# Performance work log

Measured on AMD Instinct MI355X. Metric: run time of the kernel, lower is better.

## Reference

```python
import jax, jax.numpy as jnp
import numpy as np

B, S, D = 4, 2048, 1024


def setup_inputs() -> dict:
    key = jax.random.key(0)
    ks = jax.random.split(key, 11)
    sc = 0.02
    f32 = jnp.float32
    return {
        "x1": jax.random.normal(ks[0], (B, S, D), f32),
        "x2": jax.random.normal(ks[1], (B, S, D), f32),
        "x3": jax.random.normal(ks[2], (B, S, D), f32),
        # Stacked per-modality projection weights, stored (in, out) so y = x @ W + b
        "Wq": jax.random.normal(ks[3], (3, D, D), f32) * sc,
        "bq": jax.random.normal(ks[4], (3, D), f32) * sc,
        "Wk": jax.random.normal(ks[5], (3, D, D), f32) * sc,
        "bk": jax.random.normal(ks[6], (3, D), f32) * sc,
        "Wv": jax.random.normal(ks[7], (3, D, D), f32) * sc,
        "bv": jax.random.normal(ks[8], (3, D), f32) * sc,
        "Wo": jax.random.normal(ks[9], (3, 2 * D, D), f32) * sc,
        "bo": jax.random.normal(ks[10], (3, D), f32) * sc,
    }


def reference(x1, x2, x3, Wq, bq, Wk, bk, Wv, bv, Wo, bo):
    x = jnp.stack([x1, x2, x3])                      # (3, B, S, D)
    q = jnp.einsum('mbsd,mde->mbse', x, Wq) + bq[:, None, None, :]
    k = jnp.einsum('mbsd,mde->mbse', x, Wk) + bk[:, None, None, :]
    v = jnp.einsum('mbsd,mde->mbse', x, Wv) + bv[:, None, None, :]
    scale = 1.0 / jnp.sqrt(jnp.asarray(x.shape[-1], x.dtype))
    # self-scores per modality: q_i @ k_i^T
    scores = jnp.einsum('mbsd,mbtd->mbst', q, k) * scale   # (3, B, S, S)
    attn = jax.nn.softmax(scores, axis=-1)
    # context_i = attn_i @ v_{(i+1) mod 3}  (1->2, 2->3, 3->1); dropout is eval-mode identity
    v_next = jnp.roll(v, shift=-1, axis=0)
    ctx = jnp.einsum('mbst,mbtd->mbsd', attn, v_next)      # (3, B, S, D)
    comb = jnp.concatenate([x, ctx], axis=-1)              # (3, B, S, 2D)
    out = jnp.einsum('mbsf,mfd->mbsd', comb, Wo) + bo[:, None, None, :]
    global_feature = jnp.concatenate([out[0], out[1], out[2]], axis=1)  # (B, 3S, D)
    return out[0], out[1], out[2], global_feature
```

## Files before the change

kernel.cpp:

```cpp
#include <hip/hip_runtime.h>
#include <hip/hip_bf16.h>

typedef __bf16 bf16_t;
typedef __bf16 bf16x8 __attribute__((ext_vector_type(8)));
typedef float f32x4 __attribute__((ext_vector_type(4)));

typedef __attribute__((address_space(1))) unsigned int as1_uint;
typedef __attribute__((address_space(3))) unsigned int as3_uint;

#define Bsz 4
#define Ssz 2048
#define Dsz 1024
#define BSD (Bsz * Ssz * Dsz)
#define SCALE_ 0.03125f

__device__ __forceinline__ void gll16(const void* g, void* l) {
  __builtin_amdgcn_global_load_lds((const as1_uint*)g, (as3_uint*)l, 16, 0, 0);
}

__device__ __forceinline__ void gemm_core(const bf16_t* A, const bf16_t* A2, int ksplit,
                                          int lda, int lda2,
                                          const bf16_t* Bt, int ldb,
                                          int ktiles, f32x4 acc[4][4]) {
  __shared__ __attribute__((aligned(16))) bf16_t As[128 * 64];
  __shared__ __attribute__((aligned(16))) bf16_t Bs[128 * 64];
  const int tid = threadIdx.x;
  const int wave = tid >> 6, lane = tid & 63;
  const int quad = lane >> 4, m16 = lane & 15, x7 = lane & 7;
  const int waveM = (wave >> 1) << 6, waveN = (wave & 1) << 6;
  const int srow = tid >> 3;
  const int schunk = (tid & 7) ^ ((tid >> 3) & 7);
  char* AsB = (char*)As;
  char* BsB = (char*)Bs;
  const int ldsbase = wave << 10;

  for (int kt = 0; kt < ktiles; ++kt) {
    const bf16_t* Ak = (kt < ksplit) ? (A + kt * 64) : (A2 + (kt - ksplit) * 64);
    const int ldak = (kt < ksplit) ? lda : lda2;
    const bf16_t* Bk = Bt + kt * 64;
    __syncthreads();
#pragma unroll
    for (int it = 0; it < 4; ++it)
      gll16(Ak + (size_t)(it * 32 + srow) * ldak + schunk * 8, AsB + it * 4096 + ldsbase);
#pragma unroll
    for (int it = 0; it < 4; ++it)
      gll16(Bk + (size_t)(it * 32 + srow) * ldb + schunk * 8, BsB + it * 4096 + ldsbase);
    __syncthreads();
#pragma unroll
    for (int t = 0; t < 2; ++t) {
      bf16x8 a[4], b[4];
      const int cc = t * 4 + quad;
#pragma unroll
      for (int i = 0; i < 4; ++i) {
        const int rr = waveM + i * 16 + m16;
        a[i] = *(const bf16x8*)(AsB + rr * 128 + ((cc ^ x7) << 4));
      }
#pragma unroll
      for (int j = 0; j < 4; ++j) {
        const int rr = waveN + j * 16 + m16;
        b[j] = *(const bf16x8*)(BsB + rr * 128 + ((cc ^ x7) << 4));
      }
#pragma unroll
      for (int i = 0; i < 4; ++i)
#pragma unroll
        for (int j = 0; j < 4; ++j)
          acc[i][j] = __builtin_amdgcn_mfma_f32_16x16x32_bf16(a[i], b[j], acc[i][j], 0, 0, 0);
    }
  }
}

__global__ __launch_bounds__(256, 2)
void gemm_bt_bf16(const bf16_t* __restrict__ A, long long sAz, int lda,
                  const bf16_t* __restrict__ Bt, long long sBz, int ldb,
                  const float* __restrict__ bias, int sbz,
                  bf16_t* __restrict__ C, long long sCz, int ldc,
                  int K, int rollB) {
  const int z = blockIdx.z;
  int zb = z;
  if (rollB) { const int m = z >> 2, b = z & 3; zb = ((m + 1) % 3) * Bsz + b; }
  const bf16_t* Az = A + (long long)z * sAz + (size_t)blockIdx.y * 128 * lda;
  const bf16_t* Bz = Bt + (long long)zb * sBz + (size_t)blockIdx.x * 128 * ldb;
  f32x4 acc[4][4];
  const f32x4 zero = {0.f, 0.f, 0.f, 0.f};
#pragma unroll
  for (int i = 0; i < 4; ++i)
#pragma unroll
    for (int j = 0; j < 4; ++j) acc[i][j] = zero;

  gemm_core(Az, Az, 1 << 30, lda, lda, Bz, ldb, K / 64, acc);

  const int lane = threadIdx.x & 63, wave = threadIdx.x >> 6;
  const int m0 = blockIdx.y * 128 + ((wave >> 1) << 6) + ((lane >> 4) << 2);
  const int n0 = blockIdx.x * 128 + ((wave & 1) << 6) + (lane & 15);
  bf16_t* Cz = C + (long long)z * sCz;
  const float* bz = bias ? (bias + (long long)z * sbz) : nullptr;
#pragma unroll
  for (int j = 0; j < 4; ++j) {
    const int col = n0 + j * 16;
    const float bv = bz ? bz[col] : 0.0f;
#pragma unroll
    for (int i = 0; i < 4; ++i) {
      const int row = m0 + i * 16;
#pragma unroll
      for (int r = 0; r < 4; ++r)
        Cz[(size_t)(row + r) * ldc + col] = (bf16_t)(acc[i][j][r] + bv);
    }
  }
}

__global__ __launch_bounds__(256, 2)
void gemm_out(const bf16_t* __restrict__ xb, const bf16_t* __restrict__ ctx,
              const bf16_t* __restrict__ Wot, const float* __restrict__ bo,
              float* __restrict__ out) {
  const int m = blockIdx.z;
  const bf16_t* Az = xb + (long long)m * BSD + (size_t)blockIdx.y * 128 * Dsz;
  const bf16_t* A2z = ctx + (long long)m * BSD + (size_t)blockIdx.y * 128 * Dsz;
  const bf16_t* Bz = Wot + (long long)m * (Dsz * 2 * Dsz) + (size_t)blockIdx.x * 128 * (2 * Dsz);
  f32x4 acc[4][4];
  const f32x4 zero = {0.f, 0.f, 0.f, 0.f};
#pragma unroll
  for (int i = 0; i < 4; ++i)
#pragma unroll
    for (int j = 0; j < 4; ++j) acc[i][j] = zero;

  gemm_core(Az, A2z, 16, Dsz, Dsz, Bz, 2 * Dsz, 32, acc);

  const int lane = threadIdx.x & 63, wave = threadIdx.x >> 6;
  const int m0 = blockIdx.y * 128 + ((wave >> 1) << 6) + ((lane >> 4) << 2);
  const int n0 = blockIdx.x * 128 + ((wave & 1) << 6) + (lane & 15);
  const float* bz = bo + m * Dsz;
#pragma unroll
  for (int j = 0; j < 4; ++j) {
    const int col = n0 + j * 16;
    const float bv = bz[col];
#pragma unroll
    for (int i = 0; i < 4; ++i) {
#pragma unroll
      for (int r = 0; r < 4; ++r) {
        const int row = m0 + i * 16 + r;
        const float v = acc[i][j][r] + bv;
        const int b = row >> 11, s = row & 2047;
        out[(size_t)m * BSD + (size_t)row * Dsz + col] = v;
        out[(size_t)3 * BSD + (size_t)b * (3 * Ssz * Dsz) + (size_t)(m * Ssz + s) * Dsz + col] = v;
      }
    }
  }
}

__global__ __launch_bounds__(256)
void cvt_x(const float* __restrict__ x1, const float* __restrict__ x2,
           const float* __restrict__ x3, bf16_t* __restrict__ xb) {
  const size_t i = ((size_t)blockIdx.x * 256 + threadIdx.x) * 4;
  const float* src;
  size_t off;
  if (i < (size_t)BSD)          { src = x1; off = i; }
  else if (i < (size_t)2 * BSD) { src = x2; off = i - BSD; }
  else                          { src = x3; off = i - (size_t)2 * BSD; }
  const float4 v = *(const float4*)(src + off);
  union { bf16_t h[4]; uint2 u; } o;
  o.h[0] = (bf16_t)v.x; o.h[1] = (bf16_t)v.y; o.h[2] = (bf16_t)v.z; o.h[3] = (bf16_t)v.w;
  *(uint2*)(xb + i) = o.u;
}

template <typename TIN>
__global__ __launch_bounds__(256)
void transpose_to_bf16(const TIN* __restrict__ in, bf16_t* __restrict__ out,
                       int ldin, int ldout, long long sIn, long long sOut) {
  __shared__ bf16_t Ts[64][65];
  const int t = threadIdx.x;
  const long long z = blockIdx.z;
  const TIN* inz = in + z * sIn;
  bf16_t* outz = out + z * sOut;
  const int r0 = blockIdx.y << 6, c0 = blockIdx.x << 6;
#pragma unroll
  for (int e = 0; e < 4; ++e) {
    const int idx = (e * 256 + t) * 4;
    const int rr = idx >> 6, cc = idx & 63;
    const TIN* p = inz + (size_t)(r0 + rr) * ldin + (c0 + cc);
    if constexpr (sizeof(TIN) == 4) {
      const float4 v = *(const float4*)p;
      Ts[rr][cc] = (bf16_t)v.x; Ts[rr][cc + 1] = (bf16_t)v.y;
      Ts[rr][cc + 2] = (bf16_t)v.z; Ts[rr][cc + 3] = (bf16_t)v.w;
    } else {
      union { bf16_t h[4]; uint2 u; } tmp;
      tmp.u = *(const uint2*)p;
      Ts[rr][cc] = tmp.h[0]; Ts[rr][cc + 1] = tmp.h[1];
      Ts[rr][cc + 2] = tmp.h[2]; Ts[rr][cc + 3] = tmp.h[3];
    }
  }
  __syncthreads();
#pragma unroll
  for (int e = 0; e < 4; ++e) {
    const int idx = (e * 256 + t) * 4;
    const int oc = idx >> 6, orr = idx & 63;
    union { bf16_t h[4]; uint2 u; } o4;
    o4.h[0] = Ts[orr][oc]; o4.h[1] = Ts[orr + 1][oc];
    o4.h[2] = Ts[orr + 2][oc]; o4.h[3] = Ts[orr + 3][oc];
    *(uint2*)(outz + (size_t)(c0 + oc) * ldout + (r0 + orr)) = o4.u;
  }
}

__device__ __forceinline__ unsigned bfbits(float f) {
  union { bf16_t h; unsigned short u; } c;
  c.h = (bf16_t)f;
  return (unsigned)c.u;
}

__global__ __launch_bounds__(256)
void softmax_rows(bf16_t* __restrict__ Sc) {
  const size_t row = blockIdx.x;
  uint4* p = (uint4*)(Sc + row * Ssz);
  const int t = threadIdx.x;
  const int lane = t & 63, wave = t >> 6;
  uint4 u = p[t];
  float v[8];
  v[0] = __uint_as_float(u.x << 16); v[1] = __uint_as_float(u.x & 0xffff0000u);
  v[2] = __uint_as_float(u.y << 16); v[3] = __uint_as_float(u.y & 0xffff0000u);
  v[4] = __uint_as_float(u.z << 16); v[5] = __uint_as_float(u.z & 0xffff0000u);
  v[6] = __uint_as_float(u.w << 16); v[7] = __uint_as_float(u.w & 0xffff0000u);

  float mx = v[0];
#pragma unroll
  for (int i = 1; i < 8; ++i) mx = fmaxf(mx, v[i]);
  for (int o = 32; o > 0; o >>= 1) mx = fmaxf(mx, __shfl_xor(mx, o));
  __shared__ float redm[4], reds[4];
  if (lane == 0) redm[wave] = mx;
  __syncthreads();
  mx = fmaxf(fmaxf(redm[0], redm[1]), fmaxf(redm[2], redm[3]));

  float s = 0.f;
#pragma unroll
  for (int i = 0; i < 8; ++i) { v[i] = __expf((v[i] - mx) * SCALE_); s += v[i]; }
  for (int o = 32; o > 0; o >>= 1) s += __shfl_xor(s, o);
  if (lane == 0) reds[wave] = s;
  __syncthreads();
  s = reds[0] + reds[1] + reds[2] + reds[3];
  const float inv = 1.0f / s;
#pragma unroll
  for (int i = 0; i < 8; ++i) v[i] *= inv;

  u.x = bfbits(v[0]) | (bfbits(v[1]) << 16);
  u.y = bfbits(v[2]) | (bfbits(v[3]) << 16);
  u.z = bfbits(v[4]) | (bfbits(v[5]) << 16);
  u.w = bfbits(v[6]) | (bfbits(v[7]) << 16);
  p[t] = u;
}

extern "C" void kernel_launch(void* const* d_in, const int* in_sizes, int n_in,
                              void* d_out, int out_size, void* d_ws, size_t ws_size,
                              hipStream_t stream) {
  const float* x1 = (const float*)d_in[0];
  const float* x2 = (const float*)d_in[1];
  const float* x3 = (const float*)d_in[2];
  const float* Wq = (const float*)d_in[3];
  const float* bq = (const float*)d_in[4];
  const float* Wk = (const float*)d_in[5];
  const float* bk = (const float*)d_in[6];
  const float* Wv = (const float*)d_in[7];
  const float* bv = (const float*)d_in[8];
  const float* Wo = (const float*)d_in[9];
  const float* bo = (const float*)d_in[10];

  char* ws = (char*)d_ws;
  bf16_t* xb  = (bf16_t*)(ws + 0);
  bf16_t* Wqt = (bf16_t*)(ws + 50331648);
  bf16_t* Wkt = (bf16_t*)(ws + 56623104);
  bf16_t* Wvt = (bf16_t*)(ws + 62914560);
  bf16_t* Wot = (bf16_t*)(ws + 69206016);
  bf16_t* Q   = (bf16_t*)(ws + 81788928);
  bf16_t* Kb  = (bf16_t*)(ws + 132120576);
  bf16_t* V   = (bf16_t*)(ws + 182452224);
  bf16_t* Sc  = (bf16_t*)d_out;
  bf16_t* Vt  = Q;
  bf16_t* ctx = Kb;

  cvt_x<<<24576, 256, 0, stream>>>(x1, x2, x3, xb);
  transpose_to_bf16<float><<<dim3(16, 16, 3), 256, 0, stream>>>(Wq, Wqt, 1024, 1024, 1048576LL, 1048576LL);
  transpose_to_bf16<float><<<dim3(16, 16, 3), 256, 0, stream>>>(Wk, Wkt, 1024, 1024, 1048576LL, 1048576LL);
  transpose_to_bf16<float><<<dim3(16, 16, 3), 256, 0, stream>>>(Wv, Wvt, 1024, 1024, 1048576LL, 1048576LL);
  transpose_to_bf16<float><<<dim3(16, 32, 3), 256, 0, stream>>>(Wo, Wot, 1024, 2048, 2097152LL, 2097152LL);
  const dim3 gqkv(8, 64, 3);
  gemm_bt_bf16<<<gqkv, 256, 0, stream>>>(xb, (long long)BSD, Dsz, Wqt, 1048576LL, Dsz, bq, Dsz, Q,  (long long)BSD, Dsz, Dsz, 0);
  gemm_bt_bf16<<<gqkv, 256, 0, stream>>>(xb, (long long)BSD, Dsz, Wkt, 1048576LL, Dsz, bk, Dsz, Kb, (long long)BSD, Dsz, Dsz, 0);
  gemm_bt_bf16<<<gqkv, 256, 0, stream>>>(xb, (long long)BSD, Dsz, Wvt, 1048576LL, Dsz, bv, Dsz, V,  (long long)BSD, Dsz, Dsz, 0);
  gemm_bt_bf16<<<dim3(16, 16, 12), 256, 0, stream>>>(Q, 2097152LL, Dsz, Kb, 2097152LL, Dsz, nullptr, 0, Sc, 4194304LL, Ssz, Dsz, 0);
  softmax_rows<<<24576, 256, 0, stream>>>(Sc);
  transpose_to_bf16<bf16_t><<<dim3(16, 32, 12), 256, 0, stream>>>(V, Vt, 1024, 2048, 2097152LL, 2097152LL);
  gemm_bt_bf16<<<dim3(8, 16, 12), 256, 0, stream>>>(Sc, 4194304LL, Ssz, Vt, 2097152LL, Ssz, nullptr, 0, ctx, 2097152LL, Dsz, Ssz, 1);
  gemm_out<<<dim3(8, 64, 3), 256, 0, stream>>>(xb, ctx, Wot, bo, (float*)d_out);
}
```

Baseline: 950.0 us.

## Fuse QKV projections into one GEMM with transposed V epilogue and vectorized stores

Concatenates the transposed Q/K/V weights per modality so a single launch computes all three projections, and writes V already transposed through shared memory, removing the separate V transpose kernel. Swaps the MFMA operand order so each lane holds four consecutive output columns, which lets all GEMM epilogues use vectorized 8-byte bf16 and 16-byte float stores in place of scalar stores. This costs extra shared memory and a sync in the V path, and changes the workspace buffer aliasing.

```diff
diff --git a/kernel.cpp b/kernel.cpp
--- a/kernel.cpp
+++ b/kernel.cpp
@@ -18,20 +18,23 @@
   __builtin_amdgcn_global_load_lds((const as1_uint*)g, (as3_uint*)l, 16, 0, 0);
 }
 
-__device__ __forceinline__ void gemm_core(const bf16_t* A, const bf16_t* A2, int ksplit,
+__device__ __forceinline__ unsigned bfbits(float f) {
+  union { bf16_t h; unsigned short u; } c;
+  c.h = (bf16_t)f;
+  return (unsigned)c.u;
+}
+
+__device__ __forceinline__ void gemm_core(char* AsB, char* BsB,
+                                          const bf16_t* A, const bf16_t* A2, int ksplit,
                                           int lda, int lda2,
                                           const bf16_t* Bt, int ldb,
                                           int ktiles, f32x4 acc[4][4]) {
-  __shared__ __attribute__((aligned(16))) bf16_t As[128 * 64];
-  __shared__ __attribute__((aligned(16))) bf16_t Bs[128 * 64];
   const int tid = threadIdx.x;
   const int wave = tid >> 6, lane = tid & 63;
   const int quad = lane >> 4, m16 = lane & 15, x7 = lane & 7;
   const int waveM = (wave >> 1) << 6, waveN = (wave & 1) << 6;
   const int srow = tid >> 3;
   const int schunk = (tid & 7) ^ ((tid >> 3) & 7);
-  char* AsB = (char*)As;
-  char* BsB = (char*)Bs;
   const int ldsbase = wave << 10;
 
   for (int kt = 0; kt < ktiles; ++kt) {
@@ -64,17 +67,26 @@
       for (int i = 0; i < 4; ++i)
 #pragma unroll
         for (int j = 0; j < 4; ++j)
-          acc[i][j] = __builtin_amdgcn_mfma_f32_16x16x32_bf16(a[i], b[j], acc[i][j], 0, 0, 0);
-    }
-  }
+          acc[i][j] = __builtin_amdgcn_mfma_f32_16x16x32_bf16(b[j], a[i], acc[i][j], 0, 0, 0);
+    }
+  }
+}
+
+__device__ __forceinline__ ushort4 pack4(const f32x4 v, const float4 b) {
+  ushort4 u;
+  u.x = (unsigned short)bfbits(v[0] + b.x);
+  u.y = (unsigned short)bfbits(v[1] + b.y);
+  u.z = (unsigned short)bfbits(v[2] + b.z);
+  u.w = (unsigned short)bfbits(v[3] + b.w);
+  return u;
 }
 
 __global__ __launch_bounds__(256, 2)
 void gemm_bt_bf16(const bf16_t* __restrict__ A, long long sAz, int lda,
                   const bf16_t* __restrict__ Bt, long long sBz, int ldb,
-                  const float* __restrict__ bias, int sbz,
                   bf16_t* __restrict__ C, long long sCz, int ldc,
                   int K, int rollB) {
+  __shared__ __attribute__((aligned(16))) char smem[32768];
   const int z = blockIdx.z;
   int zb = z;
   if (rollB) { const int m = z >> 2, b = z & 3; zb = ((m + 1) % 3) * Bsz + b; }
@@ -87,23 +99,89 @@
 #pragma unroll
     for (int j = 0; j < 4; ++j) acc[i][j] = zero;
 
-  gemm_core(Az, Az, 1 << 30, lda, lda, Bz, ldb, K / 64, acc);
+  gemm_core(smem, smem + 16384, Az, Az, 1 << 30, lda, lda, Bz, ldb, K / 64, acc);
 
   const int lane = threadIdx.x & 63, wave = threadIdx.x >> 6;
-  const int m0 = blockIdx.y * 128 + ((wave >> 1) << 6) + ((lane >> 4) << 2);
-  const int n0 = blockIdx.x * 128 + ((wave & 1) << 6) + (lane & 15);
+  const int Mb = blockIdx.y * 128 + ((wave >> 1) << 6) + (lane & 15);
+  const int Nb = blockIdx.x * 128 + ((wave & 1) << 6) + ((lane >> 4) << 2);
   bf16_t* Cz = C + (long long)z * sCz;
-  const float* bz = bias ? (bias + (long long)z * sbz) : nullptr;
-#pragma unroll
-  for (int j = 0; j < 4; ++j) {
-    const int col = n0 + j * 16;
-    const float bv = bz ? bz[col] : 0.0f;
-#pragma unroll
-    for (int i = 0; i < 4; ++i) {
-      const int row = m0 + i * 16;
-#pragma unroll
-      for (int r = 0; r < 4; ++r)
-        Cz[(size_t)(row + r) * ldc + col] = (bf16_t)(acc[i][j][r] + bv);
+  const float4 zb4 = {0.f, 0.f, 0.f, 0.f};
+#pragma unroll
+  for (int i = 0; i < 4; ++i) {
+    const int M = Mb + i * 16;
+#pragma unroll
+    for (int j = 0; j < 4; ++j) {
+      const int N = Nb + j * 16;
+      *(ushort4*)(Cz + (size_t)M * ldc + N) = pack4(acc[i][j], zb4);
+    }
+  }
+}
+
+__global__ __launch_bounds__(256, 2)
+void gemm_qkv(const bf16_t* __restrict__ xb, const bf16_t* __restrict__ Wqkvt,
+              const float* __restrict__ bq, const float* __restrict__ bk,
+              const float* __restrict__ bvp,
+              bf16_t* __restrict__ Q, bf16_t* __restrict__ Kb, bf16_t* __restrict__ Vt) {
+  __shared__ __attribute__((aligned(16))) char smem[34048];
+  const int m = blockIdx.z;
+  const int x = blockIdx.x;
+  const int which = x >> 3;
+  const bf16_t* Az = xb + (size_t)m * BSD + (size_t)blockIdx.y * 128 * Dsz;
+  const bf16_t* Bz = Wqkvt + (size_t)m * 3145728 + (size_t)x * 131072;
+  f32x4 acc[4][4];
+  const f32x4 zero = {0.f, 0.f, 0.f, 0.f};
+#pragma unroll
+  for (int i = 0; i < 4; ++i)
+#pragma unroll
+    for (int j = 0; j < 4; ++j) acc[i][j] = zero;
+
+  gemm_core(smem, smem + 16384, Az, Az, 1 << 30, Dsz, Dsz, Bz, Dsz, 16, acc);
+
+  const int tid = threadIdx.x;
+  const int lane = tid & 63, wave = tid >> 6;
+  const int Ml = ((wave >> 1) << 6) + (lane & 15);
+  const int Nl = ((wave & 1) << 6) + ((lane >> 4) << 2);
+  const int dseg0 = (x & 7) * 128;
+  const float* bb = (which == 0 ? bq : which == 1 ? bk : bvp) + m * Dsz;
+
+  if (which < 2) {
+    bf16_t* Cz = (which == 0 ? Q : Kb) + (size_t)m * BSD;
+#pragma unroll
+    for (int j = 0; j < 4; ++j) {
+      const int N = Nl + j * 16;
+      const float4 b4 = *(const float4*)(bb + dseg0 + N);
+#pragma unroll
+      for (int i = 0; i < 4; ++i) {
+        const int M = blockIdx.y * 128 + Ml + i * 16;
+        *(ushort4*)(Cz + (size_t)M * Dsz + dseg0 + N) = pack4(acc[i][j], b4);
+      }
+    }
+  } else {
+    unsigned short* T = (unsigned short*)smem;
+    __syncthreads();
+#pragma unroll
+    for (int j = 0; j < 4; ++j) {
+      const int N = Nl + j * 16;
+      const float4 b4 = *(const float4*)(bb + dseg0 + N);
+      const float bia[4] = {b4.x, b4.y, b4.z, b4.w};
+#pragma unroll
+      for (int i = 0; i < 4; ++i) {
+        const int M = Ml + i * 16;
+#pragma unroll
+        for (int r = 0; r < 4; ++r)
+          T[(N + r) * 132 + M] = (unsigned short)bfbits(acc[i][j][r] + bia[r]);
+      }
+    }
+    __syncthreads();
+    const int b = blockIdx.y >> 4;
+    const int s0 = (blockIdx.y & 15) * 128;
+    bf16_t* Vz = Vt + ((size_t)(m * 4 + b) * 1024 + dseg0) * Ssz;
+#pragma unroll
+    for (int e = 0; e < 16; ++e) {
+      const int idx = e * 256 + tid;
+      const int nl = idx >> 5, mc = (idx & 31) * 4;
+      const ushort4 u = *(const ushort4*)(T + nl * 132 + mc);
+      *(ushort4*)(Vz + (size_t)nl * Ssz + s0 + mc) = u;
     }
   }
 }
@@ -112,10 +190,11 @@
 void gemm_out(const bf16_t* __restrict__ xb, const bf16_t* __restrict__ ctx,
               const bf16_t* __restrict__ Wot, const float* __restrict__ bo,
               float* __restrict__ out) {
+  __shared__ __attribute__((aligned(16))) char smem[32768];
   const int m = blockIdx.z;
-  const bf16_t* Az = xb + (long long)m * BSD + (size_t)blockIdx.y * 128 * Dsz;
-  const bf16_t* A2z = ctx + (long long)m * BSD + (size_t)blockIdx.y * 128 * Dsz;
-  const bf16_t* Bz = Wot + (long long)m * (Dsz * 2 * Dsz) + (size_t)blockIdx.x * 128 * (2 * Dsz);
+  const bf16_t* Az = xb + (size_t)m * BSD + (size_t)blockIdx.y * 128 * Dsz;
+  const bf16_t* A2z = ctx + (size_t)m * BSD + (size_t)blockIdx.y * 128 * Dsz;
+  const bf16_t* Bz = Wot + (size_t)m * (Dsz * 2 * Dsz) + (size_t)blockIdx.x * 128 * (2 * Dsz);
   f32x4 acc[4][4];
   const f32x4 zero = {0.f, 0.f, 0.f, 0.f};
 #pragma unroll
@@ -123,26 +202,27 @@
 #pragma unroll
     for (int j = 0; j < 4; ++j) acc[i][j] = zero;
 
-  gemm_core(Az, A2z, 16, Dsz, Dsz, Bz, 2 * Dsz, 32, acc);
+  gemm_core(smem, smem + 16384, Az, A2z, 16, Dsz, Dsz, Bz, 2 * Dsz, 32, acc);
 
   const int lane = threadIdx.x & 63, wave = threadIdx.x >> 6;
-  const int m0 = blockIdx.y * 128 + ((wave >> 1) << 6) + ((lane >> 4) << 2);
-  const int n0 = blockIdx.x * 128 + ((wave & 1) << 6) + (lane & 15);
+  const int Mb = blockIdx.y * 128 + ((wave >> 1) << 6) + (lane & 15);
+  const int Nb = blockIdx.x * 128 + ((wave & 1) << 6) + ((lane >> 4) << 2);
   const float* bz = bo + m * Dsz;
 #pragma unroll
-  for (int j = 0; j < 4; ++j) {
-    const int col = n0 + j * 16;
-    const float bv = bz[col];
-#pragma unroll
-    for (int i = 0; i < 4; ++i) {
-#pragma unroll
-      for (int r = 0; r < 4; ++r) {
-        const int row = m0 + i * 16 + r;
-        const float v = acc[i][j][r] + bv;
-        const int b = row >> 11, s = row & 2047;
-        out[(size_t)m * BSD + (size_t)row * Dsz + col] = v;
-        out[(size_t)3 * BSD + (size_t)b * (3 * Ssz * Dsz) + (size_t)(m * Ssz + s) * Dsz + col] = v;
-      }
+  for (int i = 0; i < 4; ++i) {
+    const int M = Mb + i * 16;
+    const int b = M >> 11, s = M & 2047;
+    float* o1 = out + (size_t)m * BSD + (size_t)M * Dsz;
+    float* o2 = out + (size_t)3 * BSD + (size_t)b * (3 * Ssz * Dsz) + (size_t)(m * Ssz + s) * Dsz;
+#pragma unroll
+    for (int j = 0; j < 4; ++j) {
+      const int N = Nb + j * 16;
+      const float4 b4 = *(const float4*)(bz + N);
+      float4 o;
+      o.x = acc[i][j][0] + b4.x; o.y = acc[i][j][1] + b4.y;
+      o.z = acc[i][j][2] + b4.z; o.w = acc[i][j][3] + b4.w;
+      *(float4*)(o1 + N) = o;
+      *(float4*)(o2 + N) = o;
     }
   }
 }
@@ -162,31 +242,22 @@
   *(uint2*)(xb + i) = o.u;
 }
 
-template <typename TIN>
 __global__ __launch_bounds__(256)
-void transpose_to_bf16(const TIN* __restrict__ in, bf16_t* __restrict__ out,
+void transpose_to_bf16(const float* __restrict__ in, bf16_t* __restrict__ out,
                        int ldin, int ldout, long long sIn, long long sOut) {
   __shared__ bf16_t Ts[64][65];
   const int t = threadIdx.x;
   const long long z = blockIdx.z;
-  const TIN* inz = in + z * sIn;
+  const float* inz = in + z * sIn;
   bf16_t* outz = out + z * sOut;
   const int r0 = blockIdx.y << 6, c0 = blockIdx.x << 6;
 #pragma unroll
   for (int e = 0; e < 4; ++e) {
     const int idx = (e * 256 + t) * 4;
     const int rr = idx >> 6, cc = idx & 63;
-    const TIN* p = inz + (size_t)(r0 + rr) * ldin + (c0 + cc);
-    if constexpr (sizeof(TIN) == 4) {
-      const float4 v = *(const float4*)p;
-      Ts[rr][cc] = (bf16_t)v.x; Ts[rr][cc + 1] = (bf16_t)v.y;
-      Ts[rr][cc + 2] = (bf16_t)v.z; Ts[rr][cc + 3] = (bf16_t)v.w;
-    } else {
-      union { bf16_t h[4]; uint2 u; } tmp;
-      tmp.u = *(const uint2*)p;
-      Ts[rr][cc] = tmp.h[0]; Ts[rr][cc + 1] = tmp.h[1];
-      Ts[rr][cc + 2] = tmp.h[2]; Ts[rr][cc + 3] = tmp.h[3];
-    }
+    const float4 v = *(const float4*)(inz + (size_t)(r0 + rr) * ldin + (c0 + cc));
+    Ts[rr][cc] = (bf16_t)v.x; Ts[rr][cc + 1] = (bf16_t)v.y;
+    Ts[rr][cc + 2] = (bf16_t)v.z; Ts[rr][cc + 3] = (bf16_t)v.w;
   }
   __syncthreads();
 #pragma unroll
@@ -198,12 +269,6 @@
     o4.h[2] = Ts[orr + 2][oc]; o4.h[3] = Ts[orr + 3][oc];
     *(uint2*)(outz + (size_t)(c0 + oc) * ldout + (r0 + orr)) = o4.u;
   }
-}
-
-__device__ __forceinline__ unsigned bfbits(float f) {
-  union { bf16_t h; unsigned short u; } c;
-  c.h = (bf16_t)f;
-  return (unsigned)c.u;
 }
 
 __global__ __launch_bounds__(256)
@@ -262,30 +327,23 @@
   const float* bo = (const float*)d_in[10];
 
   char* ws = (char*)d_ws;
-  bf16_t* xb  = (bf16_t*)(ws + 0);
-  bf16_t* Wqt = (bf16_t*)(ws + 50331648);
-  bf16_t* Wkt = (bf16_t*)(ws + 56623104);
-  bf16_t* Wvt = (bf16_t*)(ws + 62914560);
-  bf16_t* Wot = (bf16_t*)(ws + 69206016);
-  bf16_t* Q   = (bf16_t*)(ws + 81788928);
-  bf16_t* Kb  = (bf16_t*)(ws + 132120576);
-  bf16_t* V   = (bf16_t*)(ws + 182452224);
-  bf16_t* Sc  = (bf16_t*)d_out;
-  bf16_t* Vt  = Q;
-  bf16_t* ctx = Kb;
+  bf16_t* xb    = (bf16_t*)(ws + 0);
+  bf16_t* Wqkvt = (bf16_t*)(ws + 50331648);
+  bf16_t* Wot   = (bf16_t*)(ws + 69206016);
+  bf16_t* Q     = (bf16_t*)(ws + 81788928);
+  bf16_t* Kb    = (bf16_t*)(ws + 132120576);
+  bf16_t* Vt    = (bf16_t*)(ws + 182452224);
+  bf16_t* Sc    = (bf16_t*)d_out;
+  bf16_t* ctx   = Q;
 
   cvt_x<<<24576, 256, 0, stream>>>(x1, x2, x3, xb);
-  transpose_to_bf16<float><<<dim3(16, 16, 3), 256, 0, stream>>>(Wq, Wqt, 1024, 1024, 1048576LL, 1048576LL);
-  transpose_to_bf16<float><<<dim3(16, 16, 3), 256, 0, stream>>>(Wk, Wkt, 1024, 1024, 1048576LL, 1048576LL);
-  transpose_to_bf16<float><<<dim3(16, 16, 3), 256, 0, stream>>>(Wv, Wvt, 1024, 1024, 1048576LL, 1048576LL);
-  transpose_to_bf16<float><<<dim3(16, 32, 3), 256, 0, stream>>>(Wo, Wot, 1024, 2048, 2097152LL, 2097152LL);
-  const dim3 gqkv(8, 64, 3);
-  gemm_bt_bf16<<<gqkv, 256, 0, stream>>>(xb, (long long)BSD, Dsz, Wqt, 1048576LL, Dsz, bq, Dsz, Q,  (long long)BSD, Dsz, Dsz, 0);
-  gemm_bt_bf16<<<gqkv, 256, 0, stream>>>(xb, (long long)BSD, Dsz, Wkt, 1048576LL, Dsz, bk, Dsz, Kb, (long long)BSD, Dsz, Dsz, 0);
-  gemm_bt_bf16<<<gqkv, 256, 0, stream>>>(xb, (long long)BSD, Dsz, Wvt, 1048576LL, Dsz, bv, Dsz, V,  (long long)BSD, Dsz, Dsz, 0);
-  gemm_bt_bf16<<<dim3(16, 16, 12), 256, 0, stream>>>(Q, 2097152LL, Dsz, Kb, 2097152LL, Dsz, nullptr, 0, Sc, 4194304LL, Ssz, Dsz, 0);
+  transpose_to_bf16<<<dim3(16, 16, 3), 256, 0, stream>>>(Wq, Wqkvt + 0,       1024, 1024, 1048576LL, 3145728LL);
+  transpose_to_bf16<<<dim3(16, 16, 3), 256, 0, stream>>>(Wk, Wqkvt + 1048576, 1024, 1024, 1048576LL, 3145728LL);
+  transpose_to_bf16<<<dim3(16, 16, 3), 256, 0, stream>>>(Wv, Wqkvt + 2097152, 1024, 1024, 1048576LL, 3145728LL);
+  transpose_to_bf16<<<dim3(16, 32, 3), 256, 0, stream>>>(Wo, Wot, 1024, 2048, 2097152LL, 2097152LL);
+  gemm_qkv<<<dim3(24, 64, 3), 256, 0, stream>>>(xb, Wqkvt, bq, bk, bv, Q, Kb, Vt);
+  gemm_bt_bf16<<<dim3(16, 16, 12), 256, 0, stream>>>(Q, 2097152LL, Dsz, Kb, 2097152LL, Dsz, Sc, 4194304LL, Ssz, Dsz, 0);
   softmax_rows<<<24576, 256, 0, stream>>>(Sc);
-  transpose_to_bf16<bf16_t><<<dim3(16, 32, 12), 256, 0, stream>>>(V, Vt, 1024, 2048, 2097152LL, 2097152LL);
-  gemm_bt_bf16<<<dim3(8, 16, 12), 256, 0, stream>>>(Sc, 4194304LL, Ssz, Vt, 2097152LL, Ssz, nullptr, 0, ctx, 2097152LL, Dsz, Ssz, 1);
+  gemm_bt_bf16<<<dim3(8, 16, 12), 256, 0, stream>>>(Sc, 4194304LL, Ssz, Vt, 2097152LL, Ssz, ctx, 2097152LL, Dsz, Ssz, 1);
   gemm_out<<<dim3(8, 64, 3), 256, 0, stream>>>(xb, ctx, Wot, bo, (float*)d_out);
 }
```

After: 871.9 us. 8.2% less time.
